# Kernel tuning notes

Measured on AMD Instinct MI355X. Metric: run time of the kernel, lower is better.

The kernel has to match this reference:

```python
import jax, jax.numpy as jnp
import numpy as np

B, N, C, T, M, H, W = 4, 500, 80, 28, 16, 800, 800
ALPHA, GAMMA, EPS = 0.25, 2.0, 1e-8
CAND_K = 10          # SimOTA candidate top-k
CTR_R = 0.25         # center-radius fraction for in-center test
CLS_W, L1_W, GIOU_W, MASK_W = 2.0, 5.0, 2.0, 5.0
IMG = 800.0


def _rand_boxes(key, shape, lo, hi):
    k1, k2 = jax.random.split(key)
    ctr = jax.random.uniform(k1, shape + (2,), minval=hi / 2, maxval=IMG - hi / 2)
    wh = jax.random.uniform(k2, shape + (2,), minval=lo, maxval=hi)
    return jnp.concatenate([ctr - wh / 2, ctr + wh / 2], axis=-1)


def setup_inputs() -> dict:
    key = jax.random.key(0)
    ks = jax.random.split(key, 6)
    return {
        'pred_logits': jax.random.normal(ks[0], (B, N, C), jnp.float32),
        'pred_boxes': _rand_boxes(ks[1], (B, N), 40.0, 320.0),
        'pred_masks': jax.random.normal(ks[2], (B, N, C, T, T), jnp.float32),
        'gt_classes': jax.random.randint(ks[3], (B, M), 0, C),
        'gt_boxes': _rand_boxes(ks[4], (B, M), 60.0, 400.0),
        'gt_masks': (jax.random.uniform(ks[5], (B, M, H, W)) > 0.5).astype(jnp.float32),
        'image_size': jnp.full((B, 4), IMG, jnp.float32),
    }


def _box_iou_union(b1, b2):
    lt = jnp.maximum(b1[..., :2], b2[..., :2])
    rb = jnp.minimum(b1[..., 2:], b2[..., 2:])
    wh = jnp.clip(rb - lt, 0.0)
    inter = wh[..., 0] * wh[..., 1]
    a1 = (b1[..., 2] - b1[..., 0]) * (b1[..., 3] - b1[..., 1])
    a2 = (b2[..., 2] - b2[..., 0]) * (b2[..., 3] - b2[..., 1])
    union = a1 + a2 - inter
    return inter / (union + EPS), union


def _giou(b1, b2):
    iou, union = _box_iou_union(b1, b2)
    lt = jnp.minimum(b1[..., :2], b2[..., :2])
    rb = jnp.maximum(b1[..., 2:], b2[..., 2:])
    wh = jnp.clip(rb - lt, 0.0)
    enc = wh[..., 0] * wh[..., 1]
    return iou - (enc - union) / (enc + EPS)


def _crop_resize(mask, box):
    # ROIAlign-style bilinear crop of a [H,W] bitmask to [T,T], then binarize (detectron2 semantics)
    x1, y1, x2, y2 = box[0], box[1], box[2], box[3]
    xs = x1 + (jnp.arange(T) + 0.5) * (x2 - x1) / T - 0.5
    ys = y1 + (jnp.arange(T) + 0.5) * (y2 - y1) / T - 0.5
    yy, xx = jnp.meshgrid(ys, xs, indexing='ij')
    s = jax.scipy.ndimage.map_coordinates(mask, [yy, xx], order=1, mode='constant')
    return (s >= 0.5).astype(jnp.float32)


def _per_image(logits, boxes, masks, gt_cls, gt_boxes, gt_masks_flat, image_size):
    # logits [N,C], boxes [N,4] xyxy, masks [N,C,T,T], gt_cls [M], gt_boxes [M,4], gt_masks_flat [M,T*T]
    cx = (boxes[:, 0] + boxes[:, 2]) * 0.5
    cy = (boxes[:, 1] + boxes[:, 3]) * 0.5
    in_box = ((cx[:, None] > gt_boxes[None, :, 0]) & (cx[:, None] < gt_boxes[None, :, 2]) &
              (cy[:, None] > gt_boxes[None, :, 1]) & (cy[:, None] < gt_boxes[None, :, 3]))
    gcx = (gt_boxes[:, 0] + gt_boxes[:, 2]) * 0.5
    gcy = (gt_boxes[:, 1] + gt_boxes[:, 3]) * 0.5
    gw = gt_boxes[:, 2] - gt_boxes[:, 0]
    gh = gt_boxes[:, 3] - gt_boxes[:, 1]
    in_ctr = ((jnp.abs(cx[:, None] - gcx[None, :]) < CTR_R * gw[None, :]) &
              (jnp.abs(cy[:, None] - gcy[None, :]) < CTR_R * gh[None, :]))
    valid = (in_box | in_ctr).any(axis=1)          # [N]
    in_both = in_box & in_ctr                       # [N,M]

    p = jax.nn.sigmoid(logits)
    neg = -jnp.log(1.0 - p + EPS) * (1.0 - ALPHA) * p ** GAMMA
    pos = -jnp.log(p + EPS) * ALPHA * (1.0 - p) ** GAMMA
    cls_cost = CLS_W * (pos - neg)[:, gt_cls]       # [N,M]

    nb = boxes / image_size
    ngb = gt_boxes / image_size
    l1_cost = L1_W * jnp.abs(nb[:, None, :] - ngb[None, :, :]).sum(-1)
    giou_cost = GIOU_W * (1.0 - _giou(nb[:, None, :], ngb[None, :, :]))

    ms = jax.nn.sigmoid(masks).reshape(N, C, T * T)
    inter = jnp.einsum('nct,mt->nmc', ms, gt_masks_flat)
    union = ms.sum(-1)[:, None, :] + gt_masks_flat.sum(-1)[None, :, None] + EPS
    dice = 1.0 - 2.0 * inter / union                # [N,M,C]
    mask_cost = MASK_W * dice[:, jnp.arange(M), gt_cls]

    cost = (cls_cost + l1_cost + giou_cost + mask_cost
            + (~in_both).astype(jnp.float32) * 1e5
            + (~valid)[:, None].astype(jnp.float32) * 1e9)
    cost = jax.lax.stop_gradient(cost)              # matcher is @no_grad

    ious, _ = _box_iou_union(boxes[:, None, :], gt_boxes[None, :, :])
    ious = jax.lax.stop_gradient(ious * valid[:, None].astype(jnp.float32))
    topk_ious, _ = jax.lax.top_k(ious.T, CAND_K)    # [M,K]
    dyn_k = jnp.clip(topk_ious.sum(-1).astype(jnp.int32), 1, None)

    def col_match(cost_col, dk):
        _, idx = jax.lax.top_k(-cost_col, CAND_K)
        sel = (jnp.arange(CAND_K) < dk).astype(jnp.float32)
        return jnp.zeros((N,), jnp.float32).at[idx].add(sel)

    matching = jax.vmap(col_match, in_axes=(1, 0), out_axes=1)(cost, dyn_k)  # [N,M]
    multi = matching.sum(axis=1) > 1
    best = jnp.argmin(cost, axis=1)
    matching = jnp.where(multi[:, None], jax.nn.one_hot(best, M, dtype=jnp.float32), matching)
    fg = (matching.sum(axis=1) > 0) & valid
    wgt = fg.astype(jnp.float32)                    # [N]
    matched = jnp.argmax(matching, axis=1)          # [N]

    tcls = gt_cls[matched]
    tgt = jax.nn.one_hot(tcls, C, dtype=jnp.float32)
    ce = jnp.maximum(logits, 0.0) - logits * tgt + jnp.log1p(jnp.exp(-jnp.abs(logits)))
    pt = p * tgt + (1.0 - p) * (1.0 - tgt)
    focal = ce * (1.0 - pt) ** GAMMA * (ALPHA * tgt + (1.0 - ALPHA) * (1.0 - tgt))
    cls_loss = (focal.sum(-1) * wgt).sum()

    mgb = ngb[matched]
    l1_loss = (jnp.abs(nb - mgb).sum(-1) * wgt).sum()
    giou_loss = ((1.0 - _giou(nb, mgb)) * wgt).sum()

    pm = ms[jnp.arange(N), tcls]                    # [N,T*T]
    gm = gt_masks_flat[matched]
    mi = (pm * gm).sum(-1)
    mu = pm.sum(-1) + gm.sum(-1) + EPS
    mask_loss = ((1.0 - 2.0 * mi / mu) * wgt).sum()
    return cls_loss, l1_loss, giou_loss, mask_loss, wgt.sum()


def reference(pred_logits, pred_boxes, pred_masks, gt_classes, gt_boxes, gt_masks, image_size):
    gm_flat = jax.vmap(jax.vmap(_crop_resize))(gt_masks, gt_boxes).reshape(B, M, T * T)
    cl, l1, gi, mk, ni = jax.vmap(_per_image)(
        pred_logits, pred_boxes, pred_masks, gt_classes, gt_boxes, gm_flat, image_size)
    n = ni.sum()
    return jnp.stack([CLS_W * cl.sum() / n, L1_W * l1.sum() / n,
                      GIOU_W * gi.sum() / n, MASK_W * mk.sum() / n])
```

## Files before the change

kernel.cpp:

```cpp
#include <hip/hip_runtime.h>
#include <math.h>

#define B_ 4
#define N_ 500
#define C_ 80
#define T_ 28
#define TT 784
#define M_ 16
#define H_ 800
#define W_ 800
#define CAND_K 10
#define EPS 1e-8f

#define OFF_GM    0
#define OFF_GSUM  (OFF_GM + B_*M_*TT)
#define OFF_COST  (OFF_GSUM + B_*M_)
#define OFF_IOUS  (OFF_COST + B_*N_*M_)
#define OFF_MATCH (OFF_IOUS + B_*N_*M_)
#define OFF_VALID (OFF_MATCH + B_*N_*M_)
#define OFF_ACC   (OFF_VALID + B_*N_)
#define WS_FLOATS (OFF_ACC + 8)

__global__ __launch_bounds__(256) void crop_kernel(
    const float* __restrict__ gtm, const float* __restrict__ gboxes,
    float* __restrict__ gm, float* __restrict__ gsum) {
  int bm = blockIdx.x;
  const float* img = gtm + (size_t)bm * (H_ * W_);
  float x1 = gboxes[bm*4+0], y1 = gboxes[bm*4+1];
  float x2 = gboxes[bm*4+2], y2 = gboxes[bm*4+3];
  float part = 0.f;
  for (int t = threadIdx.x; t < TT; t += blockDim.x) {
    int i = t / T_, j = t - i * T_;
    float y = y1 + (i + 0.5f) * (y2 - y1) / T_ - 0.5f;
    float x = x1 + (j + 0.5f) * (x2 - x1) / T_ - 0.5f;
    int y0 = (int)floorf(y), x0 = (int)floorf(x);
    float fy = y - (float)y0, fx = x - (float)x0;
    float v = 0.f;
#pragma unroll
    for (int dy = 0; dy < 2; ++dy)
#pragma unroll
      for (int dx = 0; dx < 2; ++dx) {
        int yy = y0 + dy, xx = x0 + dx;
        float w = (dy ? fy : 1.f - fy) * (dx ? fx : 1.f - fx);
        if (yy >= 0 && yy < H_ && xx >= 0 && xx < W_)
          v += w * img[yy * W_ + xx];
      }
    float g = (v >= 0.5f) ? 1.f : 0.f;
    gm[(size_t)bm * TT + t] = g;
    part += g;
  }
  __shared__ float sb[4];
  for (int off = 32; off; off >>= 1) part += __shfl_down(part, off, 64);
  int lane = threadIdx.x & 63, w = threadIdx.x >> 6;
  if (lane == 0) sb[w] = part;
  __syncthreads();
  if (threadIdx.x == 0) gsum[bm] = sb[0] + sb[1] + sb[2] + sb[3];
}

__global__ __launch_bounds__(256) void cost_kernel(
    const float* __restrict__ logits, const float* __restrict__ boxes,
    const float* __restrict__ masks, const int* __restrict__ gcls,
    const float* __restrict__ gboxes, const float* __restrict__ imgsz,
    const float* __restrict__ gm, const float* __restrict__ gsum,
    float* __restrict__ cost, float* __restrict__ ious,
    float* __restrict__ validf) {
  int blk = blockIdx.x;
  int b = blk / N_, n = blk - b * N_;
  int tid = threadIdx.x;
  __shared__ float s_ssum[M_], s_inter[M_];
  __shared__ float2 wbuf[4];
  const size_t nb_off = (size_t)(b * N_ + n);

  for (int m = 0; m < M_; ++m) {
    int gc = gcls[b * M_ + m];
    const float4* mp = (const float4*)(masks + (nb_off * C_ + gc) * TT);
    const float4* gp = (const float4*)(gm + (size_t)(b * M_ + m) * TT);
    float si = 0.f, sg = 0.f;
    if (tid < TT / 4) {
      float4 mv = mp[tid];
      float4 gv = gp[tid];
      float p0 = 1.f / (1.f + expf(-mv.x));
      float p1 = 1.f / (1.f + expf(-mv.y));
      float p2 = 1.f / (1.f + expf(-mv.z));
      float p3 = 1.f / (1.f + expf(-mv.w));
      si = p0 + p1 + p2 + p3;
      sg = p0 * gv.x + p1 * gv.y + p2 * gv.z + p3 * gv.w;
    }
    for (int off = 32; off; off >>= 1) {
      si += __shfl_down(si, off, 64);
      sg += __shfl_down(sg, off, 64);
    }
    int lane = tid & 63, w = tid >> 6;
    if (lane == 0) wbuf[w] = make_float2(si, sg);
    __syncthreads();
    if (tid == 0) {
      s_ssum[m]  = wbuf[0].x + wbuf[1].x + wbuf[2].x + wbuf[3].x;
      s_inter[m] = wbuf[0].y + wbuf[1].y + wbuf[2].y + wbuf[3].y;
    }
    __syncthreads();
  }

  float bx1 = boxes[nb_off*4+0], by1 = boxes[nb_off*4+1];
  float bx2 = boxes[nb_off*4+2], by2 = boxes[nb_off*4+3];
  float cx = (bx1 + bx2) * 0.5f, cy = (by1 + by2) * 0.5f;
  bool flag = false, in_box = false, in_ctr = false;
  float gx1 = 0, gy1 = 0, gx2 = 0, gy2 = 0;
  if (tid < M_) {
    int gi = (b * M_ + tid) * 4;
    gx1 = gboxes[gi+0]; gy1 = gboxes[gi+1]; gx2 = gboxes[gi+2]; gy2 = gboxes[gi+3];
    in_box = (cx > gx1) && (cx < gx2) && (cy > gy1) && (cy < gy2);
    float gcx = (gx1 + gx2) * 0.5f, gcy = (gy1 + gy2) * 0.5f;
    float gw = gx2 - gx1, gh = gy2 - gy1;
    in_ctr = (fabsf(cx - gcx) < 0.25f * gw) && (fabsf(cy - gcy) < 0.25f * gh);
    flag = in_box || in_ctr;
  }
  unsigned long long bal = __ballot(flag);
  bool valid = (bal != 0ULL);
  if (tid == 0) validf[nb_off] = valid ? 1.f : 0.f;

  if (tid < M_) {
    int m = tid;
    int gc = gcls[b * M_ + m];
    float lg = logits[nb_off * C_ + gc];
    float p = 1.f / (1.f + expf(-lg));
    float pos = -logf(p + EPS) * 0.25f * (1.f - p) * (1.f - p);
    float neg = -logf(1.f - p + EPS) * 0.75f * p * p;
    float ccost = 2.f * (pos - neg);
    float s0 = imgsz[b*4+0], s1 = imgsz[b*4+1], s2 = imgsz[b*4+2], s3 = imgsz[b*4+3];
    float nbx1 = bx1/s0, nby1 = by1/s1, nbx2 = bx2/s2, nby2 = by2/s3;
    float ngx1 = gx1/s0, ngy1 = gy1/s1, ngx2 = gx2/s2, ngy2 = gy2/s3;
    float l1 = 5.f * (fabsf(nbx1-ngx1) + fabsf(nby1-ngy1) +
                      fabsf(nbx2-ngx2) + fabsf(nby2-ngy2));
    float ilx = fmaxf(nbx1, ngx1), ily = fmaxf(nby1, ngy1);
    float irx = fminf(nbx2, ngx2), iry = fminf(nby2, ngy2);
    float iw = fmaxf(irx - ilx, 0.f), ih = fmaxf(iry - ily, 0.f);
    float inter = iw * ih;
    float a1 = (nbx2 - nbx1) * (nby2 - nby1);
    float a2 = (ngx2 - ngx1) * (ngy2 - ngy1);
    float uni = a1 + a2 - inter;
    float iou = inter / (uni + EPS);
    float elx = fminf(nbx1, ngx1), ely = fminf(nby1, ngy1);
    float erx = fmaxf(nbx2, ngx2), ery = fmaxf(nby2, ngy2);
    float ew = fmaxf(erx - elx, 0.f), eh = fmaxf(ery - ely, 0.f);
    float enc = ew * eh;
    float giou = iou - (enc - uni) / (enc + EPS);
    float gcost = 2.f * (1.f - giou);
    float mcost = 5.f * (1.f - 2.f * s_inter[m] / (s_ssum[m] + gsum[b*M_+m] + EPS));
    float c = ccost + l1 + gcost + mcost;
    if (!(in_box && in_ctr)) c += 1e5f;
    if (!valid) c += 1e9f;
    cost[nb_off * M_ + m] = c;
    float rlx = fmaxf(bx1, gx1), rly = fmaxf(by1, gy1);
    float rrx = fminf(bx2, gx2), rry = fminf(by2, gy2);
    float rw = fmaxf(rrx - rlx, 0.f), rh = fmaxf(rry - rly, 0.f);
    float rinter = rw * rh;
    float ra1 = (bx2 - bx1) * (by2 - by1);
    float ra2 = (gx2 - gx1) * (gy2 - gy1);
    float runi = ra1 + ra2 - rinter;
    float riou = rinter / (runi + EPS);
    ious[nb_off * M_ + m] = valid ? riou : 0.f;
  }
}

__global__ __launch_bounds__(256) void match_kernel(
    const float* __restrict__ cost, const float* __restrict__ ious,
    float* __restrict__ matching) {
  int b = blockIdx.x / M_, m = blockIdx.x - b * M_;
  int tid = threadIdx.x;
  __shared__ float cc[N_], io[N_];
  __shared__ float swv[4];
  __shared__ int swi[4];
  __shared__ int s_dk;
  for (int n = tid; n < N_; n += 256) {
    cc[n] = cost[(size_t)(b * N_ + n) * M_ + m];
    io[n] = ious[(size_t)(b * N_ + n) * M_ + m];
  }
  __syncthreads();
  int lane = tid & 63, w = tid >> 6;
  float s = 0.f;
  for (int k = 0; k < CAND_K; ++k) {
    float bv = -1e30f; int bi = 0x7fffffff;
    for (int n = tid; n < N_; n += 256) {
      float v = io[n];
      if (v > bv || (v == bv && n < bi)) { bv = v; bi = n; }
    }
    for (int off = 32; off; off >>= 1) {
      float ov = __shfl_down(bv, off, 64);
      int oi = __shfl_down(bi, off, 64);
      if (ov > bv || (ov == bv && oi < bi)) { bv = ov; bi = oi; }
    }
    if (lane == 0) { swv[w] = bv; swi[w] = bi; }
    __syncthreads();
    if (tid == 0) {
      float Bv = swv[0]; int Bi = swi[0];
      for (int ww = 1; ww < 4; ++ww)
        if (swv[ww] > Bv || (swv[ww] == Bv && swi[ww] < Bi)) { Bv = swv[ww]; Bi = swi[ww]; }
      s += Bv;
      io[Bi] = -1e30f;
    }
    __syncthreads();
  }
  if (tid == 0) {
    int dk = (int)s;
    if (dk < 1) dk = 1;
    s_dk = dk;
  }
  __syncthreads();
  int dk = s_dk;
  for (int k = 0; k < CAND_K; ++k) {
    float bv = 1e30f; int bi = 0x7fffffff;
    for (int n = tid; n < N_; n += 256) {
      float v = cc[n];
      if (v < bv || (v == bv && n < bi)) { bv = v; bi = n; }
    }
    for (int off = 32; off; off >>= 1) {
      float ov = __shfl_down(bv, off, 64);
      int oi = __shfl_down(bi, off, 64);
      if (ov < bv || (ov == bv && oi < bi)) { bv = ov; bi = oi; }
    }
    if (lane == 0) { swv[w] = bv; swi[w] = bi; }
    __syncthreads();
    if (tid == 0) {
      float Bv = swv[0]; int Bi = swi[0];
      for (int ww = 1; ww < 4; ++ww)
        if (swv[ww] < Bv || (swv[ww] == Bv && swi[ww] < Bi)) { Bv = swv[ww]; Bi = swi[ww]; }
      if (k < dk) matching[(size_t)(b * N_ + Bi) * M_ + m] = 1.f;
      cc[Bi] = 1e30f;
    }
    __syncthreads();
  }
}

__global__ __launch_bounds__(256) void loss_kernel(
    const float* __restrict__ logits, const float* __restrict__ boxes,
    const float* __restrict__ masks, const int* __restrict__ gcls,
    const float* __restrict__ gboxes, const float* __restrict__ imgsz,
    const float* __restrict__ gm, const float* __restrict__ gsum,
    const float* __restrict__ matching, const float* __restrict__ cost,
    const float* __restrict__ validf, float* __restrict__ acc) {
  int gid = blockIdx.x * blockDim.x + threadIdx.x;
  int wid = gid >> 6;
  int lane = threadIdx.x & 63;
  if (wid >= B_ * N_) return;
  int b = wid / N_, n = wid - b * N_;
  size_t nb_off = (size_t)(b * N_ + n);

  int matched = 0, fg = 0;
  if (lane == 0) {
    const float* mrow = matching + nb_off * M_;
    const float* crow = cost + nb_off * M_;
    float msum = 0.f; int first = -1;
    for (int m = 0; m < M_; ++m) {
      float v = mrow[m];
      msum += v;
      if (first < 0 && v > 0.5f) first = m;
    }
    float fgs;
    if (msum > 1.f) {
      float bv = crow[0]; int bi = 0;
      for (int m = 1; m < M_; ++m) if (crow[m] < bv) { bv = crow[m]; bi = m; }
      matched = bi; fgs = 1.f;
    } else {
      matched = (first >= 0) ? first : 0;
      fgs = msum;
    }
    fg = (fgs > 0.f && validf[nb_off] > 0.5f) ? 1 : 0;
  }
  matched = __shfl(matched, 0, 64);
  fg = __shfl(fg, 0, 64);
  if (!fg) return;

  int tcls = gcls[b * M_ + matched];
  float fsum = 0.f;
  for (int c = lane; c < C_; c += 64) {
    float l = logits[nb_off * C_ + c];
    float p = 1.f / (1.f + expf(-l));
    float tgt = (c == tcls) ? 1.f : 0.f;
    float ce = fmaxf(l, 0.f) - l * tgt + log1pf(expf(-fabsf(l)));
    float pt = p * tgt + (1.f - p) * (1.f - tgt);
    float om = 1.f - pt;
    float wf = 0.25f * tgt + 0.75f * (1.f - tgt);
    fsum += ce * om * om * wf;
  }
  float mi = 0.f, ps = 0.f;
  const float* pmrow = masks + (nb_off * C_ + tcls) * TT;
  const float* gmrow = gm + (size_t)(b * M_ + matched) * TT;
  for (int t = lane; t < TT; t += 64) {
    float pm = 1.f / (1.f + expf(-pmrow[t]));
    mi += pm * gmrow[t];
    ps += pm;
  }
  for (int off = 32; off; off >>= 1) {
    fsum += __shfl_down(fsum, off, 64);
    mi   += __shfl_down(mi, off, 64);
    ps   += __shfl_down(ps, off, 64);
  }
  if (lane == 0) {
    float bx1 = boxes[nb_off*4+0], by1 = boxes[nb_off*4+1];
    float bx2 = boxes[nb_off*4+2], by2 = boxes[nb_off*4+3];
    int gi = (b * M_ + matched) * 4;
    float gx1 = gboxes[gi+0], gy1 = gboxes[gi+1], gx2 = gboxes[gi+2], gy2 = gboxes[gi+3];
    float s0 = imgsz[b*4+0], s1 = imgsz[b*4+1], s2 = imgsz[b*4+2], s3 = imgsz[b*4+3];
    float nbx1 = bx1/s0, nby1 = by1/s1, nbx2 = bx2/s2, nby2 = by2/s3;
    float ngx1 = gx1/s0, ngy1 = gy1/s1, ngx2 = gx2/s2, ngy2 = gy2/s3;
    float l1 = fabsf(nbx1-ngx1) + fabsf(nby1-ngy1) + fabsf(nbx2-ngx2) + fabsf(nby2-ngy2);
    float ilx = fmaxf(nbx1, ngx1), ily = fmaxf(nby1, ngy1);
    float irx = fminf(nbx2, ngx2), iry = fminf(nby2, ngy2);
    float iw = fmaxf(irx - ilx, 0.f), ih = fmaxf(iry - ily, 0.f);
    float inter = iw * ih;
    float a1 = (nbx2 - nbx1) * (nby2 - nby1);
    float a2 = (ngx2 - ngx1) * (ngy2 - ngy1);
    float uni = a1 + a2 - inter;
    float iou = inter / (uni + EPS);
    float elx = fminf(nbx1, ngx1), ely = fminf(nby1, ngy1);
    float erx = fmaxf(nbx2, ngx2), ery = fmaxf(nby2, ngy2);
    float ew = fmaxf(erx - elx, 0.f), eh = fmaxf(ery - ely, 0.f);
    float enc = ew * eh;
    float giou = iou - (enc - uni) / (enc + EPS);
    float gterm = 1.f - giou;
    float mu = ps + gsum[b * M_ + matched] + EPS;
    float mterm = 1.f - 2.f * mi / mu;
    atomicAdd(&acc[0], fsum);
    atomicAdd(&acc[1], l1);
    atomicAdd(&acc[2], gterm);
    atomicAdd(&acc[3], mterm);
    atomicAdd(&acc[4], 1.f);
  }
}

__global__ void finalize_kernel(const float* __restrict__ acc, float* __restrict__ out) {
  if (threadIdx.x == 0 && blockIdx.x == 0) {
    float nf = acc[4];
    out[0] = 2.f * acc[0] / nf;
    out[1] = 5.f * acc[1] / nf;
    out[2] = 2.f * acc[2] / nf;
    out[3] = 5.f * acc[3] / nf;
  }
}

extern "C" void kernel_launch(void* const* d_in, const int* in_sizes, int n_in,
                              void* d_out, int out_size, void* d_ws, size_t ws_size,
                              hipStream_t stream) {
  const float* logits = (const float*)d_in[0];
  const float* boxes  = (const float*)d_in[1];
  const float* masks  = (const float*)d_in[2];
  const int*   gcls   = (const int*)d_in[3];
  const float* gboxes = (const float*)d_in[4];
  const float* gtm    = (const float*)d_in[5];
  const float* imgsz  = (const float*)d_in[6];

  float* ws       = (float*)d_ws;
  float* gm       = ws + OFF_GM;
  float* gsum     = ws + OFF_GSUM;
  float* cost     = ws + OFF_COST;
  float* ious     = ws + OFF_IOUS;
  float* matching = ws + OFF_MATCH;
  float* validf   = ws + OFF_VALID;
  float* acc      = ws + OFF_ACC;

  hipMemsetAsync(matching, 0, (size_t)B_ * N_ * M_ * sizeof(float), stream);
  hipMemsetAsync(acc, 0, 8 * sizeof(float), stream);

  crop_kernel<<<B_ * M_, 256, 0, stream>>>(gtm, gboxes, gm, gsum);
  cost_kernel<<<B_ * N_, 256, 0, stream>>>(logits, boxes, masks, gcls, gboxes,
                                           imgsz, gm, gsum, cost, ious, validf);
  match_kernel<<<B_ * M_, 256, 0, stream>>>(cost, ious, matching);
  loss_kernel<<<(B_ * N_ * 64 + 255) / 256, 256, 0, stream>>>(
      logits, boxes, masks, gcls, gboxes, imgsz, gm, gsum, matching, cost,
      validf, acc);
  finalize_kernel<<<1, 64, 0, stream>>>(acc, (float*)d_out);
}
```

Baseline: 694.3 us.

## Assign GT masks per wave in cost kernel and fold memsets into kernels

The cost kernel now gives each wavefront its own subset of GT masks and reduces with wave shuffles only. This removes the per-mask block-wide barriers and shared-memory combine. The separate memset launches are replaced by zeroing the accumulator in the crop kernel and the matching matrix inside the match kernel's load loop. The trade-off is less parallelism per mask, since each wave loops over 196 float4 elements, in exchange for fewer syncs and launches.

```diff
diff --git a/kernel.cpp b/kernel.cpp
--- a/kernel.cpp
+++ b/kernel.cpp
@@ -23,7 +23,8 @@
 
 __global__ __launch_bounds__(256) void crop_kernel(
     const float* __restrict__ gtm, const float* __restrict__ gboxes,
-    float* __restrict__ gm, float* __restrict__ gsum) {
+    float* __restrict__ gm, float* __restrict__ gsum, float* __restrict__ acc) {
+  if (blockIdx.x == 0 && threadIdx.x < 8) acc[threadIdx.x] = 0.f;
   int bm = blockIdx.x;
   const float* img = gtm + (size_t)bm * (H_ * W_);
   float x1 = gboxes[bm*4+0], y1 = gboxes[bm*4+1];
@@ -67,38 +68,32 @@
   int blk = blockIdx.x;
   int b = blk / N_, n = blk - b * N_;
   int tid = threadIdx.x;
+  int lane = tid & 63, wave = tid >> 6;
   __shared__ float s_ssum[M_], s_inter[M_];
-  __shared__ float2 wbuf[4];
   const size_t nb_off = (size_t)(b * N_ + n);
 
-  for (int m = 0; m < M_; ++m) {
+  for (int m = wave; m < M_; m += 4) {
     int gc = gcls[b * M_ + m];
     const float4* mp = (const float4*)(masks + (nb_off * C_ + gc) * TT);
     const float4* gp = (const float4*)(gm + (size_t)(b * M_ + m) * TT);
     float si = 0.f, sg = 0.f;
-    if (tid < TT / 4) {
-      float4 mv = mp[tid];
-      float4 gv = gp[tid];
+    for (int t = lane; t < TT / 4; t += 64) {
+      float4 mv = mp[t];
+      float4 gv = gp[t];
       float p0 = 1.f / (1.f + expf(-mv.x));
       float p1 = 1.f / (1.f + expf(-mv.y));
       float p2 = 1.f / (1.f + expf(-mv.z));
       float p3 = 1.f / (1.f + expf(-mv.w));
-      si = p0 + p1 + p2 + p3;
-      sg = p0 * gv.x + p1 * gv.y + p2 * gv.z + p3 * gv.w;
+      si += p0 + p1 + p2 + p3;
+      sg += p0 * gv.x + p1 * gv.y + p2 * gv.z + p3 * gv.w;
     }
     for (int off = 32; off; off >>= 1) {
       si += __shfl_down(si, off, 64);
       sg += __shfl_down(sg, off, 64);
     }
-    int lane = tid & 63, w = tid >> 6;
-    if (lane == 0) wbuf[w] = make_float2(si, sg);
-    __syncthreads();
-    if (tid == 0) {
-      s_ssum[m]  = wbuf[0].x + wbuf[1].x + wbuf[2].x + wbuf[3].x;
-      s_inter[m] = wbuf[0].y + wbuf[1].y + wbuf[2].y + wbuf[3].y;
-    }
-    __syncthreads();
-  }
+    if (lane == 0) { s_ssum[m] = si; s_inter[m] = sg; }
+  }
+  __syncthreads();
 
   float bx1 = boxes[nb_off*4+0], by1 = boxes[nb_off*4+1];
   float bx2 = boxes[nb_off*4+2], by2 = boxes[nb_off*4+3];
@@ -174,6 +169,7 @@
   for (int n = tid; n < N_; n += 256) {
     cc[n] = cost[(size_t)(b * N_ + n) * M_ + m];
     io[n] = ious[(size_t)(b * N_ + n) * M_ + m];
+    matching[(size_t)(b * N_ + n) * M_ + m] = 0.f;
   }
   __syncthreads();
   int lane = tid & 63, w = tid >> 6;
@@ -358,10 +354,7 @@
   float* validf   = ws + OFF_VALID;
   float* acc      = ws + OFF_ACC;
 
-  hipMemsetAsync(matching, 0, (size_t)B_ * N_ * M_ * sizeof(float), stream);
-  hipMemsetAsync(acc, 0, 8 * sizeof(float), stream);
-
-  crop_kernel<<<B_ * M_, 256, 0, stream>>>(gtm, gboxes, gm, gsum);
+  crop_kernel<<<B_ * M_, 256, 0, stream>>>(gtm, gboxes, gm, gsum, acc);
   cost_kernel<<<B_ * N_, 256, 0, stream>>>(logits, boxes, masks, gcls, gboxes,
                                            imgsz, gm, gsum, cost, ious, validf);
   match_kernel<<<B_ * M_, 256, 0, stream>>>(cost, ious, matching);
```

After: 685.1 us. No clear change (-1.3%).
